# Optimization experiments

Hardware: AMD Instinct MI355X
Metric: run time of the kernel (lower is better)

The kernel has to match this reference:

```python
import jax, jax.numpy as jnp
import numpy as np

ITERATIONS = 4


def setup_inputs() -> dict:
    key = jax.random.key(0)
    x = jax.random.normal(key, (256, 512, 256), dtype=jnp.float32)
    return {"x": x}


def reference(x):
    # axis == 1 branch of the torch module (default)
    N, len_m, len_d = x.shape
    m = jnp.mean(x, axis=1, keepdims=True)          # [N, 1, D]
    xn = x - m                                      # [N, M, D]
    # sigma = xn^T xn / (M - 1)  -> [N, D, D]
    sigma = jnp.einsum('nmd,nme->nde', xn, xn) / (len_m - 1)

    # trace-normalized Newton-Schulz iteration for inverse sqrt
    trace = jnp.trace(sigma, axis1=-2, axis2=-1)[:, None, None]  # [N, 1, 1]
    sigma_norm = sigma / trace
    P = jnp.broadcast_to(jnp.eye(len_d, dtype=x.dtype), (N, len_d, len_d))
    for _ in range(ITERATIONS):
        P3 = P @ P @ P                              # matrix_power(P, 3), batched
        P = 1.5 * P - 0.5 * (P3 @ sigma_norm)
    wm = P / jnp.sqrt(trace)                        # whitening matrix [N, D, D]

    decorrelated = xn @ wm                          # [N, M, D]
    return decorrelated
```

## Files before the change

### kernel.cpp

```cpp
#include <hip/hip_runtime.h>
#include <stdint.h>

#define Nn 256
#define Mm 512
#define Dd 256

typedef unsigned short u16;
typedef unsigned int u32;
typedef __attribute__((ext_vector_type(8))) short bf16x8;
typedef __attribute__((ext_vector_type(4))) float f32x4;

#define AGPR_W(dst, src) asm volatile("v_accvgpr_write_b32 %0, %1" : "=a"(dst) : "v"(src))
#define AGPR_R(dst, src) asm volatile("v_accvgpr_read_b32 %0, %1" : "=v"(dst) : "a"(src))

__device__ __forceinline__ u16 f2b(float f) {
    unsigned u = __float_as_uint(f);
    return (u16)((u + 0x7FFFu + ((u >> 16) & 1u)) >> 16);
}
__device__ __forceinline__ float b2f(u16 h) {
    return __uint_as_float(((unsigned)h) << 16);
}
__device__ __forceinline__ u32 pk2(float lo, float hi) {
    return (u32)f2b(lo) | ((u32)f2b(hi) << 16);
}
__device__ __forceinline__ void glds16(const u16* g, u16* l) {
    __builtin_amdgcn_global_load_lds((const __attribute__((address_space(1))) void*)g,
                                     (__attribute__((address_space(3))) void*)l, 16, 0, 0);
}

__global__ __launch_bounds__(256) void mean_part_kernel(const float* __restrict__ x,
                                                        float* __restrict__ meanPart) {
    const int bid = blockIdx.x;
    const int n = bid >> 2, c = bid & 3;
    const int tid = threadIdx.x;
    const float* xb = x + (size_t)n * Mm * Dd + (size_t)c * 128 * Dd;
    float a0 = 0.f, a1 = 0.f, a2 = 0.f, a3 = 0.f;
    for (int m = 0; m < 128; m += 4) {
        a0 += xb[(m + 0) * Dd + tid];
        a1 += xb[(m + 1) * Dd + tid];
        a2 += xb[(m + 2) * Dd + tid];
        a3 += xb[(m + 3) * Dd + tid];
    }
    meanPart[((size_t)n * 4 + c) * Dd + tid] = a0 + a1 + a2 + a3;
}

__global__ __launch_bounds__(256) void center_tr_kernel(const float* __restrict__ x,
                                                        const float* __restrict__ meanPart,
                                                        u16* __restrict__ xn,
                                                        u16* __restrict__ xnT) {
    __shared__ float meanS[Dd];
    __shared__ u16 tileS[64 * 66];
    const int bid = blockIdx.x;
    const int n = bid >> 3, mt = bid & 7;
    const int tid = threadIdx.x;

    const float* mp = meanPart + (size_t)n * 4 * Dd;
    meanS[tid] = (mp[tid] + mp[Dd + tid] + mp[2 * Dd + tid] + mp[3 * Dd + tid]) * (1.0f / Mm);
    __syncthreads();

    const float* xb = x + (size_t)n * Mm * Dd;
    u16* xnb = xn + (size_t)n * Mm * Dd;
    u16* xtb = xnT + (size_t)n * Dd * Mm;
    const int mrow = tid >> 4, dq = tid & 15;
    const int tx2 = (tid & 31) * 2, ty = tid >> 5;

    for (int dt = 0; dt < Dd / 64; ++dt) {
        #pragma unroll
        for (int rr = 0; rr < 4; ++rr) {
            int ml = mrow + 16 * rr;
            int m = mt * 64 + ml;
            int d = dt * 64 + dq * 4;
            float4 v = *(const float4*)(xb + (size_t)m * Dd + d);
            float4 mu = *(const float4*)(meanS + d);
            u16 b0 = f2b(v.x - mu.x), b1 = f2b(v.y - mu.y);
            u16 b2 = f2b(v.z - mu.z), b3 = f2b(v.w - mu.w);
            u32 lo = (u32)b0 | ((u32)b1 << 16);
            u32 hi = (u32)b2 | ((u32)b3 << 16);
            *(uint2*)(xnb + (size_t)m * Dd + d) = make_uint2(lo, hi);
            tileS[(dq * 4 + 0) * 66 + ml] = b0;
            tileS[(dq * 4 + 1) * 66 + ml] = b1;
            tileS[(dq * 4 + 2) * 66 + ml] = b2;
            tileS[(dq * 4 + 3) * 66 + ml] = b3;
        }
        __syncthreads();
        #pragma unroll
        for (int r = 0; r < 8; ++r) {
            int dl = r * 8 + ty;
            u32 w = *(const u32*)(tileS + dl * 66 + tx2);
            *(u32*)(xtb + (size_t)(dt * 64 + dl) * Mm + mt * 64 + tx2) = w;
        }
        __syncthreads();
    }
}

__global__ __launch_bounds__(256) void sigma_kernel(const u16* __restrict__ xnT,
                                                    float* __restrict__ sigma) {
    __shared__ u16 sA[128 * 32];
    __shared__ u16 sB[128 * 32];
    const int bid = blockIdx.x;
    const int xcd = bid & 7, slot = bid >> 3;
    const int t = slot & 3;
    const int n = ((slot >> 2) << 3) | xcd;
    const int tr = t >> 1, tc = t & 1;
    const int tid = threadIdx.x;
    const int lane = tid & 63, wave = tid >> 6;
    const int wr = wave >> 1, wc = wave & 1;
    const int l15 = lane & 15, quad = lane >> 4;
    const int row0 = tid >> 2, q = tid & 3;
    const int wb8 = (tid & 192) * 8;

    const u16* base = xnT + (size_t)n * Dd * Mm;
    const u16* gA = base + (size_t)(tr * 128) * Mm;
    const u16* gB = base + (size_t)(tc * 128) * Mm;

    f32x4 acc[4][4];
    #pragma unroll
    for (int i = 0; i < 4; ++i)
        #pragma unroll
        for (int j = 0; j < 4; ++j) acc[i][j] = (f32x4){0.f, 0.f, 0.f, 0.f};

    for (int kk = 0; kk < Mm; kk += 32) {
        glds16(gA + (size_t)row0 * Mm + kk + q * 8, sA + wb8);
        glds16(gA + (size_t)(row0 + 64) * Mm + kk + q * 8, sA + 2048 + wb8);
        glds16(gB + (size_t)row0 * Mm + kk + q * 8, sB + wb8);
        glds16(gB + (size_t)(row0 + 64) * Mm + kk + q * 8, sB + 2048 + wb8);
        __syncthreads();
        bf16x8 a[4], b[4];
        #pragma unroll
        for (int i = 0; i < 4; ++i) a[i] = *(const bf16x8*)(sA + (wr * 64 + i * 16 + l15) * 32 + quad * 8);
        #pragma unroll
        for (int j = 0; j < 4; ++j) b[j] = *(const bf16x8*)(sB + (wc * 64 + j * 16 + l15) * 32 + quad * 8);
        #pragma unroll
        for (int i = 0; i < 4; ++i)
            #pragma unroll
            for (int j = 0; j < 4; ++j)
                acc[i][j] = __builtin_amdgcn_mfma_f32_16x16x32_bf16(a[i], b[j], acc[i][j], 0, 0, 0);
        __syncthreads();
    }

    float* sg = sigma + (size_t)n * Dd * Dd;
    #pragma unroll
    for (int i = 0; i < 4; ++i)
        #pragma unroll
        for (int j = 0; j < 4; ++j)
            #pragma unroll
            for (int r = 0; r < 4; ++r) {
                int row = tr * 128 + wr * 64 + i * 16 + quad * 4 + r;
                int col = tc * 128 + wc * 64 + j * 16 + l15;
                sg[row * Dd + col] = acc[i][j][r];
            }
}

__device__ __forceinline__ bf16x8 ldP(const u16* Plds, int row, int ch) {
    return *(const bf16x8*)(Plds + row * 256 + ((ch ^ (row & 7)) << 3));
}

__global__ __launch_bounds__(1024, 4) void ns_chain_kernel(const float* __restrict__ sigma,
                                                           u16* __restrict__ Wg,
                                                           u16* __restrict__ Sh,
                                                           u16* __restrict__ Sl) {
    __shared__ __align__(16) u16 lds[81920];
    u16* Plds = lds;
    u16* strips = lds + 65536;
    u16* sQ = strips;
    u16* sA = strips;
    u16* sS = strips + 8192;

    const int n = blockIdx.x, tid = threadIdx.x;
    const int lane = tid & 63, wave = tid >> 6;
    const int l15 = lane & 15, quad = lane >> 4;
    const int wr = wave >> 2, wc = wave & 3;
    const int wr8 = wave >> 1, wc2 = wave & 1;

    const float* sg = sigma + (size_t)n * 65536;
    u16* shp = Sh + (size_t)n * 65536;
    u16* slp = Sl + (size_t)n * 65536;

    float* red = (float*)strips;
    if (tid < 256) red[tid] = sg[tid * 257];
    __syncthreads();
    for (int s = 128; s > 0; s >>= 1) {
        if (tid < s) red[tid] += red[tid + s];
        __syncthreads();
    }
    const float inv = 1.0f / red[0];
    const float rtr = sqrtf(511.0f * inv);

    #pragma unroll 4
    for (int itp = 0; itp < 16; ++itp) {
        int idx = itp * 4096 + tid * 4;
        float4 v = *(const float4*)(sg + idx);
        int row = idx >> 8, col = idx & 255;
        float s0 = v.x * inv, s1 = v.y * inv, s2 = v.z * inv, s3 = v.w * inv;
        u16 h0 = f2b(s0), h1 = f2b(s1), h2 = f2b(s2), h3 = f2b(s3);
        *(uint2*)(shp + idx) = make_uint2((u32)h0 | ((u32)h1 << 16), (u32)h2 | ((u32)h3 << 16));
        u16 e0 = f2b(s0 - b2f(h0)), e1 = f2b(s1 - b2f(h1));
        u16 e2 = f2b(s2 - b2f(h2)), e3 = f2b(s3 - b2f(h3));
        *(uint2*)(slp + idx) = make_uint2((u32)e0 | ((u32)e1 << 16), (u32)e2 | ((u32)e3 << 16));
        u16 p0 = f2b(((row == col + 0) ? 1.5f : 0.f) - 0.5f * s0);
        u16 p1 = f2b(((row == col + 1) ? 1.5f : 0.f) - 0.5f * s1);
        u16 p2 = f2b(((row == col + 2) ? 1.5f : 0.f) - 0.5f * s2);
        u16 p3 = f2b(((row == col + 3) ? 1.5f : 0.f) - 0.5f * s3);
        int pa = row * 256 + (((col >> 3) ^ (row & 7)) << 3) + (col & 7);
        *(uint2*)(Plds + pa) = make_uint2((u32)p0 | ((u32)p1 << 16), (u32)p2 | ((u32)p3 << 16));
    }
    __syncthreads();

    const u16* sBase = (wave < 8) ? shp : slp;
    const int w8 = wave & 7;
    const int cl_st = w8 * 16 + (lane >> 2);
    const int gch_st = (lane & 3) ^ (cl_st & 3);
    u16* sDst = sS + ((wave < 8) ? 0 : 4096) + w8 * 512 + lane * 8;

    #pragma unroll 1
    for (int it = 0; it < 3; ++it) {
        const bool last = (it == 2);
        u32 qbf[32];
        u32 p3a[32];

        #pragma unroll
        for (int h = 0; h < 2; ++h) {
            f32x4 acc1[4][2];
            #pragma unroll
            for (int i = 0; i < 4; ++i)
                #pragma unroll
                for (int jj = 0; jj < 2; ++jj) acc1[i][jj] = (f32x4){0.f, 0.f, 0.f, 0.f};
            #pragma unroll
            for (int s = 0; s < 8; ++s) {
                bf16x8 b0 = ldP(Plds, wc * 64 + (2 * h + 0) * 16 + l15, s * 4 + quad);
                bf16x8 b1 = ldP(Plds, wc * 64 + (2 * h + 1) * 16 + l15, s * 4 + quad);
                #pragma unroll
                for (int i = 0; i < 4; ++i) {
                    bf16x8 a = ldP(Plds, wr * 64 + i * 16 + l15, s * 4 + quad);
                    acc1[i][0] = __builtin_amdgcn_mfma_f32_16x16x32_bf16(a, b0, acc1[i][0], 0, 0, 0);
                    acc1[i][1] = __builtin_amdgcn_mfma_f32_16x16x32_bf16(a, b1, acc1[i][1], 0, 0, 0);
                }
            }
            #pragma unroll
            for (int i = 0; i < 4; ++i)
                #pragma unroll
                for (int jj = 0; jj < 2; ++jj)
                    #pragma unroll
                    for (int rh = 0; rh < 2; ++rh)
                        qbf[(i * 4 + 2 * h + jj) * 2 + rh] =
                            pk2(acc1[i][jj][2 * rh], acc1[i][jj][2 * rh + 1]);
        }

        #pragma unroll
        for (int jp = 0; jp < 4; ++jp) {
            if (wc == jp) {
                #pragma unroll
                for (int i = 0; i < 4; ++i)
                    #pragma unroll
                    for (int j = 0; j < 4; ++j) {
                        int cl = j * 16 + l15;
                        int k0 = wr * 64 + i * 16 + quad * 4;
                        int addr = cl * 256 + (((k0 >> 3) ^ (cl & 7)) << 3) + (k0 & 7);
                        *(uint2*)(sQ + addr) = make_uint2(qbf[(i * 4 + j) * 2], qbf[(i * 4 + j) * 2 + 1]);
                    }
            }
            __syncthreads();
            f32x4 acc2[4];
            #pragma unroll
            for (int jj = 0; jj < 4; ++jj) acc2[jj] = (f32x4){0.f, 0.f, 0.f, 0.f};
            #pragma unroll
            for (int s = 0; s < 8; ++s) {
                bf16x8 a = ldP(Plds, wave * 16 + l15, s * 4 + quad);
                #pragma unroll
                for (int jj = 0; jj < 4; ++jj) {
                    int cl = jj * 16 + l15;
                    bf16x8 b = *(const bf16x8*)(sQ + cl * 256 + (((s * 4 + quad) ^ (cl & 7)) << 3));
                    acc2[jj] = __builtin_amdgcn_mfma_f32_16x16x32_bf16(a, b, acc2[jj], 0, 0, 0);
                }
            }
            #pragma unroll
            for (int jj = 0; jj < 4; ++jj)
                #pragma unroll
                for (int rh = 0; rh < 2; ++rh)
                    AGPR_W(p3a[(jp * 4 + jj) * 2 + rh], pk2(acc2[jj][2 * rh], acc2[jj][2 * rh + 1]));
            __syncthreads();
        }

        uint4 greg = *(const uint4*)(sBase + (size_t)cl_st * 256 + gch_st * 8);
        #pragma unroll 1
        for (int jc = 0; jc < 2; ++jc) {
            f32x4 acc3[2][4];
            #pragma unroll
            for (int i16 = 0; i16 < 2; ++i16)
                #pragma unroll
                for (int j = 0; j < 4; ++j) acc3[i16][j] = (f32x4){0.f, 0.f, 0.f, 0.f};
            #pragma unroll
            for (int s = 0; s < 8; ++s) {
                #pragma unroll
                for (int jjh = 0; jjh < 2; ++jjh) {
                    int jjsrc = (s & 1) * 2 + jjh;
                    int kloc = jjh * 16 + l15;
                    int ch = kloc >> 3, k7 = kloc & 7;
                    #pragma unroll
                    for (int rh = 0; rh < 2; ++rh) {
                        u32 wv;
                        AGPR_R(wv, p3a[((s >> 1) * 4 + jjsrc) * 2 + rh]);
                        #pragma unroll
                        for (int bit = 0; bit < 2; ++bit) {
                            int row = wave * 16 + quad * 4 + 2 * rh + bit;
                            int sw = (row ^ (row >> 2)) & 3;
                            sA[row * 32 + ((ch ^ sw) << 3) + k7] =
                                (u16)(bit ? (wv >> 16) : (wv & 0xffffu));
                        }
                    }
                }
                *(uint4*)sDst = greg;
                if (!(jc == 1 && s == 7)) {
                    int t = jc * 8 + s + 1;
                    int jcn = t >> 3, sn = t & 7;
                    greg = *(const uint4*)(sBase + (size_t)(jcn * 128 + cl_st) * 256 + sn * 32 + gch_st * 8);
                }
                asm volatile("s_waitcnt lgkmcnt(0)" ::: "memory");
                __builtin_amdgcn_s_barrier();
                {
                    bf16x8 a[2];
                    #pragma unroll
                    for (int i16 = 0; i16 < 2; ++i16) {
                        int ar = wr8 * 32 + i16 * 16 + l15;
                        int asw = (ar ^ (ar >> 2)) & 3;
                        a[i16] = *(const bf16x8*)(sA + ar * 32 + ((quad ^ asw) << 3));
                    }
                    #pragma unroll
                    for (int j = 0; j < 4; ++j) {
                        int cl = wc2 * 64 + j * 16 + l15;
                        int co = cl * 32 + ((quad ^ (cl & 3)) << 3);
                        bf16x8 bh = *(const bf16x8*)(sS + co);
                        bf16x8 bl = *(const bf16x8*)(sS + 4096 + co);
                        #pragma unroll
                        for (int i16 = 0; i16 < 2; ++i16)
                            acc3[i16][j] = __builtin_amdgcn_mfma_f32_16x16x32_bf16(a[i16], bh, acc3[i16][j], 0, 0, 0);
                        #pragma unroll
                        for (int i16 = 0; i16 < 2; ++i16)
                            acc3[i16][j] = __builtin_amdgcn_mfma_f32_16x16x32_bf16(a[i16], bl, acc3[i16][j], 0, 0, 0);
                    }
                }
                asm volatile("s_waitcnt lgkmcnt(0)" ::: "memory");
                __builtin_amdgcn_s_barrier();
            }
            #pragma unroll
            for (int i16 = 0; i16 < 2; ++i16)
                #pragma unroll
                for (int j = 0; j < 4; ++j)
                    #pragma unroll
                    for (int r = 0; r < 4; ++r) {
                        int row = wr8 * 32 + i16 * 16 + quad * 4 + r;
                        int col = jc * 128 + wc2 * 64 + j * 16 + l15;
                        int pa = row * 256 + (((col >> 3) ^ (row & 7)) << 3) + (col & 7);
                        float pv = 1.5f * b2f(Plds[pa]) - 0.5f * acc3[i16][j][r];
                        if (last) Wg[(size_t)n * 65536 + row * 256 + col] = f2b(pv * rtr);
                        else Plds[pa] = f2b(pv);
                    }
        }
        __syncthreads();
    }
}

__global__ __launch_bounds__(256) void final_gemm(const u16* __restrict__ xn,
                                                  const u16* __restrict__ Wh,
                                                  float* __restrict__ out) {
    __shared__ u16 sA[128 * 32];
    __shared__ u16 sB[128 * 32];
    const int bid = blockIdx.x;
    const int xcd = bid & 7, slot = bid >> 3;
    const int t = slot & 7;
    const int n = ((slot >> 3) << 3) | xcd;
    const int tr = t >> 1, tc = t & 1;
    const int tid = threadIdx.x;
    const int lane = tid & 63, wave = tid >> 6;
    const int wr = wave >> 1, wc = wave & 1;
    const int l15 = lane & 15, quad = lane >> 4;
    const int row0 = tid >> 2, q = tid & 3;
    const int wb8 = (tid & 192) * 8;

    const u16* gA = xn + (size_t)n * Mm * Dd + (size_t)(tr * 128) * Dd;
    const u16* gB = Wh + (size_t)n * Dd * Dd + (size_t)(tc * 128) * Dd;

    f32x4 acc[4][4];
    #pragma unroll
    for (int i = 0; i < 4; ++i)
        #pragma unroll
        for (int j = 0; j < 4; ++j) acc[i][j] = (f32x4){0.f, 0.f, 0.f, 0.f};

    for (int kk = 0; kk < Dd; kk += 32) {
        glds16(gA + (size_t)row0 * Dd + kk + q * 8, sA + wb8);
        glds16(gA + (size_t)(row0 + 64) * Dd + kk + q * 8, sA + 2048 + wb8);
        glds16(gB + (size_t)row0 * Dd + kk + q * 8, sB + wb8);
        glds16(gB + (size_t)(row0 + 64) * Dd + kk + q * 8, sB + 2048 + wb8);
        __syncthreads();
        bf16x8 a[4], b[4];
        #pragma unroll
        for (int i = 0; i < 4; ++i) a[i] = *(const bf16x8*)(sA + (wr * 64 + i * 16 + l15) * 32 + quad * 8);
        #pragma unroll
        for (int j = 0; j < 4; ++j) b[j] = *(const bf16x8*)(sB + (wc * 64 + j * 16 + l15) * 32 + quad * 8);
        #pragma unroll
        for (int i = 0; i < 4; ++i)
            #pragma unroll
            for (int j = 0; j < 4; ++j)
                acc[i][j] = __builtin_amdgcn_mfma_f32_16x16x32_bf16(a[i], b[j], acc[i][j], 0, 0, 0);
        __syncthreads();
    }

    float* ob = out + (size_t)n * Mm * Dd;
    #pragma unroll
    for (int i = 0; i < 4; ++i)
        #pragma unroll
        for (int j = 0; j < 4; ++j)
            #pragma unroll
            for (int r = 0; r < 4; ++r) {
                int row = tr * 128 + wr * 64 + i * 16 + quad * 4 + r;
                int col = tc * 128 + wc * 64 + j * 16 + l15;
                ob[(size_t)row * Dd + col] = acc[i][j][r];
            }
}

extern "C" void kernel_launch(void* const* d_in, const int* in_sizes, int n_in,
                              void* d_out, int out_size, void* d_ws, size_t ws_size,
                              hipStream_t stream) {
    const float* x = (const float*)d_in[0];
    float* out = (float*)d_out;
    char* ws = (char*)d_ws;
    const size_t MB32 = 33554432;

    u16* xn = (u16*)(ws + 0);
    u16* xnT = (u16*)(ws + 2 * MB32);
    u16* W = (u16*)(ws + 2 * MB32);
    float* sigma = (float*)(ws + 4 * MB32);
    u16* Sh = (u16*)(ws + 6 * MB32);
    u16* Sl = (u16*)(ws + 7 * MB32);
    float* meanPart = (float*)(ws + 9 * MB32);

    mean_part_kernel<<<Nn * 4, 256, 0, stream>>>(x, meanPart);
    center_tr_kernel<<<Nn * 8, 256, 0, stream>>>(x, meanPart, xn, xnT);
    sigma_kernel<<<Nn * 4, 256, 0, stream>>>(xnT, sigma);
    ns_chain_kernel<<<Nn, 1024, 0, stream>>>(sigma, W, Sh, Sl);
    final_gemm<<<Nn * 8, 256, 0, stream>>>(xn, W, out);
}
```

Baseline: 626.7 us.

## Compute P^2 strips on demand, double-buffer sigma prefetch, coalesce W store

Instead of each wave computing a 64x64 block of P*P up front and holding it in 32 registers, each wave now computes its 16-row strip of the current 64-column slab of P*P right before it is used, which drops the qbf register array and the serialized per-column-group store. The global prefetch of sigma strips is double-buffered with two registers, fetching two steps ahead to hide more latency. The final whitening matrix is written back into LDS and then copied out with coalesced 16-byte stores instead of scattered 2-byte global writes. The trade-off is that P rows are loaded from LDS more often, and the wider prefetch raises register use.

```diff
diff --git a/kernel.cpp b/kernel.cpp
--- a/kernel.cpp
+++ b/kernel.cpp
@@ -169,7 +169,6 @@
     const int n = blockIdx.x, tid = threadIdx.x;
     const int lane = tid & 63, wave = tid >> 6;
     const int l15 = lane & 15, quad = lane >> 4;
-    const int wr = wave >> 2, wc = wave & 3;
     const int wr8 = wave >> 1, wc2 = wave & 1;
 
     const float* sg = sigma + (size_t)n * 65536;
@@ -215,73 +214,58 @@
     #pragma unroll 1
     for (int it = 0; it < 3; ++it) {
         const bool last = (it == 2);
-        u32 qbf[32];
         u32 p3a[32];
 
         #pragma unroll
-        for (int h = 0; h < 2; ++h) {
-            f32x4 acc1[4][2];
-            #pragma unroll
-            for (int i = 0; i < 4; ++i)
-                #pragma unroll
-                for (int jj = 0; jj < 2; ++jj) acc1[i][jj] = (f32x4){0.f, 0.f, 0.f, 0.f};
-            #pragma unroll
-            for (int s = 0; s < 8; ++s) {
-                bf16x8 b0 = ldP(Plds, wc * 64 + (2 * h + 0) * 16 + l15, s * 4 + quad);
-                bf16x8 b1 = ldP(Plds, wc * 64 + (2 * h + 1) * 16 + l15, s * 4 + quad);
-                #pragma unroll
-                for (int i = 0; i < 4; ++i) {
-                    bf16x8 a = ldP(Plds, wr * 64 + i * 16 + l15, s * 4 + quad);
-                    acc1[i][0] = __builtin_amdgcn_mfma_f32_16x16x32_bf16(a, b0, acc1[i][0], 0, 0, 0);
-                    acc1[i][1] = __builtin_amdgcn_mfma_f32_16x16x32_bf16(a, b1, acc1[i][1], 0, 0, 0);
-                }
-            }
-            #pragma unroll
-            for (int i = 0; i < 4; ++i)
-                #pragma unroll
-                for (int jj = 0; jj < 2; ++jj)
-                    #pragma unroll
-                    for (int rh = 0; rh < 2; ++rh)
-                        qbf[(i * 4 + 2 * h + jj) * 2 + rh] =
-                            pk2(acc1[i][jj][2 * rh], acc1[i][jj][2 * rh + 1]);
-        }
-
-        #pragma unroll
         for (int jp = 0; jp < 4; ++jp) {
-            if (wc == jp) {
-                #pragma unroll
-                for (int i = 0; i < 4; ++i)
-                    #pragma unroll
-                    for (int j = 0; j < 4; ++j) {
-                        int cl = j * 16 + l15;
-                        int k0 = wr * 64 + i * 16 + quad * 4;
-                        int addr = cl * 256 + (((k0 >> 3) ^ (cl & 7)) << 3) + (k0 & 7);
-                        *(uint2*)(sQ + addr) = make_uint2(qbf[(i * 4 + j) * 2], qbf[(i * 4 + j) * 2 + 1]);
-                    }
+            {
+                f32x4 acc1[4];
+                #pragma unroll
+                for (int jj = 0; jj < 4; ++jj) acc1[jj] = (f32x4){0.f, 0.f, 0.f, 0.f};
+                #pragma unroll
+                for (int s = 0; s < 8; ++s) {
+                    bf16x8 a = ldP(Plds, wave * 16 + l15, s * 4 + quad);
+                    #pragma unroll
+                    for (int jj = 0; jj < 4; ++jj) {
+                        bf16x8 b = ldP(Plds, jp * 64 + jj * 16 + l15, s * 4 + quad);
+                        acc1[jj] = __builtin_amdgcn_mfma_f32_16x16x32_bf16(a, b, acc1[jj], 0, 0, 0);
+                    }
+                }
+                #pragma unroll
+                for (int jj = 0; jj < 4; ++jj) {
+                    int cl = jj * 16 + l15;
+                    int k0 = wave * 16 + quad * 4;
+                    int addr = cl * 256 + (((k0 >> 3) ^ (cl & 7)) << 3) + (k0 & 7);
+                    *(uint2*)(sQ + addr) = make_uint2(pk2(acc1[jj][0], acc1[jj][1]),
+                                                      pk2(acc1[jj][2], acc1[jj][3]));
+                }
             }
             __syncthreads();
-            f32x4 acc2[4];
-            #pragma unroll
-            for (int jj = 0; jj < 4; ++jj) acc2[jj] = (f32x4){0.f, 0.f, 0.f, 0.f};
-            #pragma unroll
-            for (int s = 0; s < 8; ++s) {
-                bf16x8 a = ldP(Plds, wave * 16 + l15, s * 4 + quad);
-                #pragma unroll
-                for (int jj = 0; jj < 4; ++jj) {
-                    int cl = jj * 16 + l15;
-                    bf16x8 b = *(const bf16x8*)(sQ + cl * 256 + (((s * 4 + quad) ^ (cl & 7)) << 3));
-                    acc2[jj] = __builtin_amdgcn_mfma_f32_16x16x32_bf16(a, b, acc2[jj], 0, 0, 0);
-                }
+            {
+                f32x4 acc2[4];
+                #pragma unroll
+                for (int jj = 0; jj < 4; ++jj) acc2[jj] = (f32x4){0.f, 0.f, 0.f, 0.f};
+                #pragma unroll
+                for (int s = 0; s < 8; ++s) {
+                    bf16x8 a = ldP(Plds, wave * 16 + l15, s * 4 + quad);
+                    #pragma unroll
+                    for (int jj = 0; jj < 4; ++jj) {
+                        int cl = jj * 16 + l15;
+                        bf16x8 b = *(const bf16x8*)(sQ + cl * 256 + (((s * 4 + quad) ^ (cl & 7)) << 3));
+                        acc2[jj] = __builtin_amdgcn_mfma_f32_16x16x32_bf16(a, b, acc2[jj], 0, 0, 0);
+                    }
+                }
+                #pragma unroll
+                for (int jj = 0; jj < 4; ++jj)
+                    #pragma unroll
+                    for (int rh = 0; rh < 2; ++rh)
+                        AGPR_W(p3a[(jp * 4 + jj) * 2 + rh], pk2(acc2[jj][2 * rh], acc2[jj][2 * rh + 1]));
             }
-            #pragma unroll
-            for (int jj = 0; jj < 4; ++jj)
-                #pragma unroll
-                for (int rh = 0; rh < 2; ++rh)
-                    AGPR_W(p3a[(jp * 4 + jj) * 2 + rh], pk2(acc2[jj][2 * rh], acc2[jj][2 * rh + 1]));
             __syncthreads();
         }
 
-        uint4 greg = *(const uint4*)(sBase + (size_t)cl_st * 256 + gch_st * 8);
+        uint4 gregA = *(const uint4*)(sBase + (size_t)cl_st * 256 + gch_st * 8);
+        uint4 gregB = *(const uint4*)(sBase + (size_t)cl_st * 256 + 32 + gch_st * 8);
         #pragma unroll 1
         for (int jc = 0; jc < 2; ++jc) {
             f32x4 acc3[2][4];
@@ -309,11 +293,20 @@
                         }
                     }
                 }
-                *(uint4*)sDst = greg;
-                if (!(jc == 1 && s == 7)) {
-                    int t = jc * 8 + s + 1;
-                    int jcn = t >> 3, sn = t & 7;
-                    greg = *(const uint4*)(sBase + (size_t)(jcn * 128 + cl_st) * 256 + sn * 32 + gch_st * 8);
+                if ((s & 1) == 0) {
+                    *(uint4*)sDst = gregA;
+                    int t2 = jc * 8 + s + 2;
+                    if (t2 < 16) {
+                        int jcn = t2 >> 3, sn = t2 & 7;
+                        gregA = *(const uint4*)(sBase + (size_t)(jcn * 128 + cl_st) * 256 + sn * 32 + gch_st * 8);
+                    }
+                } else {
+                    *(uint4*)sDst = gregB;
+                    int t2 = jc * 8 + s + 2;
+                    if (t2 < 16) {
+                        int jcn = t2 >> 3, sn = t2 & 7;
+                        gregB = *(const uint4*)(sBase + (size_t)(jcn * 128 + cl_st) * 256 + sn * 32 + gch_st * 8);
+                    }
                 }
                 asm volatile("s_waitcnt lgkmcnt(0)" ::: "memory");
                 __builtin_amdgcn_s_barrier();
@@ -352,11 +345,19 @@
                         int col = jc * 128 + wc2 * 64 + j * 16 + l15;
                         int pa = row * 256 + (((col >> 3) ^ (row & 7)) << 3) + (col & 7);
                         float pv = 1.5f * b2f(Plds[pa]) - 0.5f * acc3[i16][j][r];
-                        if (last) Wg[(size_t)n * 65536 + row * 256 + col] = f2b(pv * rtr);
-                        else Plds[pa] = f2b(pv);
+                        Plds[pa] = f2b(last ? pv * rtr : pv);
                     }
         }
         __syncthreads();
+    }
+
+    u16* wg = Wg + (size_t)n * 65536;
+    #pragma unroll
+    for (int q = 0; q < 8; ++q) {
+        int f = q * 1024 + tid;
+        int row = f >> 5, ch = f & 31;
+        uint4 v = *(const uint4*)(Plds + row * 256 + ((ch ^ (row & 7)) << 3));
+        *(uint4*)(wg + row * 256 + ch * 8) = v;
     }
 }
 
```

New measurement: 583.3 us. 6.9% less time.
